# Optimization experiments

Hardware: AMD Instinct MI355X
Metric: run time of the kernel (lower is better)

The kernel has to match this reference:

```python
import jax, jax.numpy as jnp
import numpy as np

B, T, C = 4, 2048, 1024
H, HKV, D = 8, 4, 128          # query heads, kv heads, head dim (C = H*D)
RATIO = 4                       # csa_compress_ratio -> block size
G = T // RATIO                  # number of compressed blocks (T divisible by RATIO)
HI, DI = 8, 64                  # indexer heads / head dim
TOPK = 64                       # index_topk blocks selected per query
ROPE_DIM = 64                   # partial RoPE applied to last ROPE_DIM dims of D
THETA = 160000.0                # compress_rope_theta
RANK = 512                      # grouped output projection rank (o_groups=1)
NEG = -1e30


def rmsnorm(x):
    return x * jax.lax.rsqrt(jnp.mean(jnp.square(x), axis=-1, keepdims=True) + 1e-6)


def rope_tables(pos):
    half = ROPE_DIM // 2
    inv_freq = 1.0 / (THETA ** (jnp.arange(half, dtype=jnp.float32) / half))
    ang = pos.astype(jnp.float32)[:, None] * inv_freq[None, :]   # [P, half]
    return jnp.cos(ang), jnp.sin(ang)


def partial_rope(x, cos, sin):
    # x: [..., P, heads, D]; rotate only the last ROPE_DIM dims
    x_nope, x_rope = x[..., :-ROPE_DIM], x[..., -ROPE_DIM:]
    x1, x2 = jnp.split(x_rope, 2, axis=-1)
    c = cos[:, None, :]  # [P,1,half] broadcast over heads
    s = sin[:, None, :]
    rot = jnp.concatenate([x1 * c - x2 * s, x1 * s + x2 * c], axis=-1)
    return jnp.concatenate([x_nope, rot], axis=-1)


def gated_compress(x, Wk, Wv, Wg, ape, n_head, head_dim):
    # Learned gated softmax pooling over fixed blocks of RATIO tokens.
    k = (x @ Wk).reshape(B, G, RATIO, n_head, head_dim)
    v = (x @ Wv).reshape(B, G, RATIO, n_head, head_dim)
    g = (x @ Wg).reshape(B, G, RATIO, n_head, head_dim) + ape[None, None]
    w = jax.nn.softmax(g, axis=2)
    return (k * w).sum(axis=2), (v * w).sum(axis=2)  # [B,G,h,d]


def setup_inputs() -> dict:
    key = jax.random.key(0)
    ks = jax.random.split(key, 11)
    s = 0.02
    def w(k, shape):
        return jax.random.normal(k, shape, jnp.float32) * s
    return {
        "x": jax.random.normal(ks[0], (B, T, C), jnp.float32),
        "Wq": w(ks[1], (C, H * D)),
        "Wck": w(ks[2], (C, HKV * D)),
        "Wcv": w(ks[3], (C, HKV * D)),
        "Wcg": w(ks[4], (C, HKV * D)),
        "ape_c": jnp.zeros((RATIO, HKV, D), jnp.float32),
        "Wiq": w(ks[5], (C, HI * DI)),
        "Wik": w(ks[6], (C, HI * DI)),
        "Wig": w(ks[7], (C, HI * DI)),
        "ape_i": jnp.zeros((RATIO, HI, DI), jnp.float32),
        "Wa": w(ks[8], (1, RANK, C)),
        "Wb": w(ks[9], (RANK, C)),
    }


def reference(x, Wq, Wck, Wcv, Wcg, ape_c, Wiq, Wik, Wig, ape_i, Wa, Wb):
    group_ends = jnp.arange(RATIO - 1, T, RATIO)                 # [G]
    causal = group_ends[None, :] <= jnp.arange(T)[:, None]       # [T,G]

    # --- LightningIndexer: select TOPK compressed blocks per query token ---
    ki = (x @ Wik).reshape(B, G, RATIO, HI, DI)
    gi = (x @ Wig).reshape(B, G, RATIO, HI, DI) + ape_i[None, None]
    wi = jax.nn.softmax(gi, axis=2)
    ikeys = rmsnorm((ki * wi).sum(axis=2))                       # [B,G,HI,DI]
    iq = rmsnorm((x @ Wiq).reshape(B, T, HI, DI))
    isc = jnp.einsum('bthd,bghd->bhtg', iq, ikeys) * (DI ** -0.5)
    isc = isc.mean(axis=1)                                       # [B,T,G]
    isc = jnp.where(causal[None], isc, NEG)
    sel = jax.lax.top_k(isc, TOPK)[1]                            # [B,T,TOPK]
    mask = jnp.zeros((B, T, G), dtype=bool).at[
        jnp.arange(B)[:, None, None], jnp.arange(T)[None, :, None], sel
    ].set(True)
    mask = mask & causal[None]                                   # [B,T,G]

    # --- Compressed KV + partial RoPE ---
    ck, cv = gated_compress(x, Wck, Wcv, Wcg, ape_c, HKV, D)     # [B,G,HKV,D]
    cos_q, sin_q = rope_tables(jnp.arange(T))
    cos_k, sin_k = rope_tables(group_ends)
    q = partial_rope((x @ Wq).reshape(B, T, H, D), cos_q, sin_q)
    ck = partial_rope(ck, cos_k, sin_k)

    # --- GQA attention over selected compressed blocks ---
    rep = H // HKV
    ck_r = jnp.repeat(ck, rep, axis=2)                           # [B,G,H,D]
    cv_r = jnp.repeat(cv, rep, axis=2)
    scores = jnp.einsum('bthd,bghd->bhtg', q, ck_r) * (D ** -0.5)
    m = mask[:, None]                                            # [B,1,T,G]
    attw = jax.nn.softmax(jnp.where(m, scores, NEG), axis=-1) * m
    attn = jnp.einsum('bhtg,bghd->bthd', attw, cv_r).reshape(B, T, C)

    # --- GroupedOutputProjection (o_groups=1, low-rank) ---
    r = jnp.einsum('btgd,grd->btgr', attn.reshape(B, T, 1, C), Wa).reshape(B, T, RANK)
    return rmsnorm(r) @ Wb
```

## Files before the change

### kernel.cpp

```cpp
#include <hip/hip_runtime.h>
#include <hip/hip_bf16.h>
#include <math.h>

constexpr int kB = 4, kT = 2048, kC = 1024;
constexpr int kH = 8, kHKV = 4, kD = 128;
constexpr int kRATIO = 4, kG = 512;
constexpr int kHI = 8, kDI = 64;
constexpr int kTOPK = 64, kRANK = 512;
constexpr float kTHETA = 160000.0f;
constexpr float kNEG = -1e30f;

constexpr int NTOT = 2560;
constexpr int Q_OFF = 0;
constexpr int CK_OFF = 1024;
constexpr int CV_OFF = 1536;
constexpr int CG_OFF = 2048;

constexpr int PLD = 1536;
constexpr int P_IQ = 0, P_KI = 512, P_GI = 1024;

typedef short short8 __attribute__((ext_vector_type(8)));
typedef float floatx4 __attribute__((ext_vector_type(4)));

__device__ inline float waveReduceSum(float v) {
    #pragma unroll
    for (int m = 32; m > 0; m >>= 1) v += __shfl_xor(v, m, 64);
    return v;
}
__device__ inline double waveReduceSumD(double v) {
    #pragma unroll
    for (int m = 32; m > 0; m >>= 1) v += __shfl_xor(v, m, 64);
    return v;
}
__device__ inline float waveReduceMax(float v) {
    #pragma unroll
    for (int m = 32; m > 0; m >>= 1) v = fmaxf(v, __shfl_xor(v, m, 64));
    return v;
}

__device__ inline unsigned short f2bf(float f) {
    union { float f; unsigned int u; } v; v.f = f;
    unsigned int r = v.u + 0x7FFFu + ((v.u >> 16) & 1u);
    return (unsigned short)(r >> 16);
}
__device__ inline float bf2f(unsigned short h) {
    union { unsigned int u; float f; } v; v.u = ((unsigned int)h) << 16;
    return v.f;
}

__global__ __launch_bounds__(256) void split_rows_kernel(
    const float* __restrict__ in, unsigned short* __restrict__ out,
    int K, int kshift, const float* __restrict__ rowScale)
{
    int idx = blockIdx.x * 256 + threadIdx.x;
    int row = idx >> kshift;
    int kc = (idx & ((1 << kshift) - 1)) << 2;
    float4 v = *(const float4*)(in + (size_t)row * K + kc);
    if (rowScale) {
        float s = rowScale[row];
        v.x *= s; v.y *= s; v.z *= s; v.w *= s;
    }
    unsigned short h[4], l[4];
    float vv[4] = {v.x, v.y, v.z, v.w};
    #pragma unroll
    for (int i = 0; i < 4; ++i) {
        h[i] = f2bf(vv[i]);
        l[i] = f2bf(vv[i] - bf2f(h[i]));
    }
    size_t ob = (size_t)row * (2 * K);
    uint2 hw, lw;
    hw.x = (unsigned)h[0] | ((unsigned)h[1] << 16);
    hw.y = (unsigned)h[2] | ((unsigned)h[3] << 16);
    lw.x = (unsigned)l[0] | ((unsigned)l[1] << 16);
    lw.y = (unsigned)l[2] | ((unsigned)l[3] << 16);
    *(uint2*)(out + ob + kc) = hw;
    *(uint2*)(out + ob + K + kc) = lw;
}

__global__ __launch_bounds__(256) void transpose_split_kernel(
    const float* __restrict__ W, int N, int K, unsigned short* __restrict__ Wt)
{
    __shared__ float Ws[64][68];
    int k0 = blockIdx.x * 64, n0 = blockIdx.y * 64;
    int tid = threadIdx.x;
    #pragma unroll
    for (int it = 0; it < 4; ++it) {
        int krow = (tid >> 4) + it * 16;
        float4 v = *(const float4*)(W + (size_t)(k0 + krow) * N + n0 + (tid & 15) * 4);
        *(float4*)&Ws[krow][(tid & 15) * 4] = v;
    }
    __syncthreads();
    #pragma unroll
    for (int it = 0; it < 2; ++it) {
        int idx = tid + it * 256;
        int nrow = idx >> 3;
        int kc8 = (idx & 7) * 8;
        unsigned short h[8], l[8];
        #pragma unroll
        for (int j = 0; j < 8; ++j) {
            float v = Ws[kc8 + j][nrow];
            h[j] = f2bf(v);
            l[j] = f2bf(v - bf2f(h[j]));
        }
        size_t ob = (size_t)(n0 + nrow) * (2 * K) + k0;
        uint4 hw, lw;
        hw.x = (unsigned)h[0] | ((unsigned)h[1] << 16);
        hw.y = (unsigned)h[2] | ((unsigned)h[3] << 16);
        hw.z = (unsigned)h[4] | ((unsigned)h[5] << 16);
        hw.w = (unsigned)h[6] | ((unsigned)h[7] << 16);
        lw.x = (unsigned)l[0] | ((unsigned)l[1] << 16);
        lw.y = (unsigned)l[2] | ((unsigned)l[3] << 16);
        lw.z = (unsigned)l[4] | ((unsigned)l[5] << 16);
        lw.w = (unsigned)l[6] | ((unsigned)l[7] << 16);
        *(uint4*)(Wt + ob + kc8) = hw;
        *(uint4*)(Wt + ob + K + kc8) = lw;
    }
}

#define TSTRIDE 40

__global__ __launch_bounds__(256) void gemm_mfma_kernel(
    const unsigned short* __restrict__ A,
    const unsigned short* __restrict__ B,
    float* __restrict__ C, int ldc, int Kin)
{
    __shared__ unsigned short As[128 * TSTRIDE];
    __shared__ unsigned short Bs[128 * TSTRIDE];
    const int tid = threadIdx.x;
    const int n0 = blockIdx.x * 128, m0 = blockIdx.y * 128;
    const int w = tid >> 6, lane = tid & 63;
    const int q = lane >> 4, r = lane & 15;
    const int wm = (w & 1) * 64, wn = (w >> 1) * 64;
    const int lda = 2 * Kin, ldb = 2 * Kin;
    const int srow = tid >> 2;
    const int sko = (tid & 3) * 8;

    floatx4 acc[4][4] = {};
    const int KT = 3 * Kin;
    for (int k0 = 0; k0 < KT; k0 += 32) {
        int ka = (k0 < 2 * Kin) ? k0 : k0 - 2 * Kin;
        int kb = (k0 < Kin) ? k0 : k0 - Kin;
        __syncthreads();
        #pragma unroll
        for (int rep = 0; rep < 2; ++rep) {
            int row = srow + rep * 64;
            uint4 av = *(const uint4*)(A + (size_t)(m0 + row) * lda + ka + sko);
            uint4 bv = *(const uint4*)(B + (size_t)(n0 + row) * ldb + kb + sko);
            *(uint4*)&As[row * TSTRIDE + sko] = av;
            *(uint4*)&Bs[row * TSTRIDE + sko] = bv;
        }
        __syncthreads();
        short8 af[4], bf[4];
        #pragma unroll
        for (int i = 0; i < 4; ++i)
            af[i] = *(const short8*)&As[(wm + i * 16 + r) * TSTRIDE + q * 8];
        #pragma unroll
        for (int j = 0; j < 4; ++j)
            bf[j] = *(const short8*)&Bs[(wn + j * 16 + r) * TSTRIDE + q * 8];
        #pragma unroll
        for (int i = 0; i < 4; ++i)
            #pragma unroll
            for (int j = 0; j < 4; ++j)
                acc[i][j] = __builtin_amdgcn_mfma_f32_16x16x32_bf16(
                    af[i], bf[j], acc[i][j], 0, 0, 0);
    }
    #pragma unroll
    for (int i = 0; i < 4; ++i)
        #pragma unroll
        for (int j = 0; j < 4; ++j)
            #pragma unroll
            for (int reg = 0; reg < 4; ++reg)
                C[(size_t)(m0 + wm + i * 16 + q * 4 + reg) * ldc
                  + n0 + wn + j * 16 + r] = acc[i][j][reg];
}

__global__ __launch_bounds__(256) void rope_q_kernel(float* __restrict__ Y)
{
    int idx = blockIdx.x * 256 + threadIdx.x;
    int j = idx & 31;
    int rest = idx >> 5;
    int h = rest & 7;  rest >>= 3;
    int t = rest & (kT - 1);
    int b = rest >> 11;
    size_t base = (size_t)(b * kT + t) * NTOT + Q_OFF + h * kD;
    float inv_freq = powf(kTHETA, -(float)j * (1.0f / 32.0f));
    float ang = (float)t * inv_freq;
    float c = cosf(ang), s = sinf(ang);
    float x1 = Y[base + 64 + j];
    float x2 = Y[base + 96 + j];
    Y[base + 64 + j] = x1 * c - x2 * s;
    Y[base + 96 + j] = x1 * s + x2 * c;
}

__global__ __launch_bounds__(128) void compress_c_kernel(
    const float* __restrict__ Y, const float* __restrict__ ape_c,
    float* __restrict__ ck, float* __restrict__ cv)
{
    int bid = blockIdx.x;
    int h = bid & 3;
    int g = (bid >> 2) & (kG - 1);
    int b = bid >> 11;
    int d = threadIdx.x;
    float kv[kRATIO], vv[kRATIO], gv[kRATIO];
    #pragma unroll
    for (int r = 0; r < kRATIO; ++r) {
        size_t row = (size_t)(b * kT + g * kRATIO + r) * NTOT;
        kv[r] = Y[row + CK_OFF + h * kD + d];
        vv[r] = Y[row + CV_OFF + h * kD + d];
        gv[r] = Y[row + CG_OFF + h * kD + d] + ape_c[(r * kHKV + h) * kD + d];
    }
    float m = fmaxf(fmaxf(gv[0], gv[1]), fmaxf(gv[2], gv[3]));
    float ka = 0.f, va = 0.f, den = 0.f;
    #pragma unroll
    for (int r = 0; r < kRATIO; ++r) {
        float e = expf(gv[r] - m);
        den += e;
        ka += kv[r] * e;
        va += vv[r] * e;
    }
    ka /= den; va /= den;
    size_t obase = ((size_t)(b * kG + g) * kHKV + h) * kD;
    cv[obase + d] = va;
    __shared__ float cks[kD];
    cks[d] = ka;
    __syncthreads();
    int pos = 4 * g + 3;
    float out;
    if (d < 64) {
        out = cks[d];
    } else if (d < 96) {
        int j = d - 64;
        float inv_freq = powf(kTHETA, -(float)j * (1.0f / 32.0f));
        float ang = (float)pos * inv_freq;
        out = cks[d] * cosf(ang) - cks[d + 32] * sinf(ang);
    } else {
        int j = d - 96;
        float inv_freq = powf(kTHETA, -(float)j * (1.0f / 32.0f));
        float ang = (float)pos * inv_freq;
        out = cks[d - 32] * sinf(ang) + cks[d] * cosf(ang);
    }
    ck[obase + d] = out;
}

__global__ __launch_bounds__(256) void concat_w_kernel(
    const float* __restrict__ Wiq, const float* __restrict__ Wik,
    const float* __restrict__ Wig, float* __restrict__ Wcat)
{
    int idx = blockIdx.x * 256 + threadIdx.x;
    int row = idx / 384;
    int col = (idx - row * 384) * 4;
    float4 v;
    if (col < 512)       v = *(const float4*)(Wiq + (size_t)row * 512 + col);
    else if (col < 1024) v = *(const float4*)(Wik + (size_t)row * 512 + col - 512);
    else                 v = *(const float4*)(Wig + (size_t)row * 512 + col - 1024);
    *(float4*)(Wcat + (size_t)row * PLD + col) = v;
}

#define PBM 128
#define PBN 64
#define PBK 16

__global__ __launch_bounds__(256) void proj_f64_kernel(
    const float* __restrict__ x, const float* __restrict__ W,
    double* __restrict__ P)
{
    __shared__ double As[PBK][129];
    __shared__ double Bs[PBK][68];
    const int tid = threadIdx.x;
    const int bx = blockIdx.x, by = blockIdx.y;
    const int tx = tid & 15, ty = tid >> 4;
    const int ar = tid >> 1;
    const int ak = (tid & 1) * 8;
    const int br = tid >> 4;
    const int bc = tid & 15;
    const float* Ap = x + (size_t)(by * PBM + ar) * kC + ak;
    const float* Bp = W + (size_t)br * PLD + bx * PBN + bc;
    double acc[8][4] = {};
    for (int k0 = 0; k0 < kC; k0 += PBK) {
        float4 a0 = *(const float4*)(Ap + k0);
        float4 a1 = *(const float4*)(Ap + k0 + 4);
        const float* bp = Bp + (size_t)k0 * PLD;
        float b0 = bp[0], b1 = bp[16], b2 = bp[32], b3 = bp[48];
        __syncthreads();
        As[ak + 0][ar] = (double)a0.x;
        As[ak + 1][ar] = (double)a0.y;
        As[ak + 2][ar] = (double)a0.z;
        As[ak + 3][ar] = (double)a0.w;
        As[ak + 4][ar] = (double)a1.x;
        As[ak + 5][ar] = (double)a1.y;
        As[ak + 6][ar] = (double)a1.z;
        As[ak + 7][ar] = (double)a1.w;
        Bs[br][bc]      = (double)b0;
        Bs[br][bc + 16] = (double)b1;
        Bs[br][bc + 32] = (double)b2;
        Bs[br][bc + 48] = (double)b3;
        __syncthreads();
        #pragma unroll
        for (int kk = 0; kk < PBK; ++kk) {
            double a[8], b[4];
            #pragma unroll
            for (int i = 0; i < 8; ++i) a[i] = As[kk][ty * 8 + i];
            #pragma unroll
            for (int j = 0; j < 4; ++j) b[j] = Bs[kk][tx + 16 * j];
            #pragma unroll
            for (int i = 0; i < 8; ++i)
                #pragma unroll
                for (int j = 0; j < 4; ++j)
                    acc[i][j] = fma(a[i], b[j], acc[i][j]);
        }
    }
    #pragma unroll
    for (int i = 0; i < 8; ++i)
        #pragma unroll
        for (int j = 0; j < 4; ++j)
            P[(size_t)(by * PBM + ty * 8 + i) * PLD + bx * PBN + tx + 16 * j] = acc[i][j];
}

__global__ __launch_bounds__(64) void gate_i_kernel(
    const double* __restrict__ P, const float* __restrict__ ape_i,
    double* __restrict__ ikeys64)
{
    int bid = blockIdx.x;
    int h = bid & 7;
    int g = (bid >> 3) & (kG - 1);
    int b = bid >> 12;
    int lane = threadIdx.x;
    double kk[kRATIO], gg[kRATIO];
    #pragma unroll
    for (int r = 0; r < kRATIO; ++r) {
        size_t row = (size_t)(b * kT + g * kRATIO + r) * PLD;
        kk[r] = P[row + P_KI + h * kDI + lane];
        gg[r] = P[row + P_GI + h * kDI + lane] + (double)ape_i[(r * kHI + h) * kDI + lane];
    }
    double m = fmax(fmax(gg[0], gg[1]), fmax(gg[2], gg[3]));
    double acc = 0.0, den = 0.0;
    #pragma unroll
    for (int r = 0; r < kRATIO; ++r) {
        double e = exp(gg[r] - m);
        den += e;
        acc += kk[r] * e;
    }
    acc /= den;
    double ss = waveReduceSumD(acc * acc);
    double scale = 1.0 / sqrt(ss * (1.0 / kDI) + 1e-6);
    ikeys64[((size_t)(b * kG + g) * kHI + h) * kDI + lane] = acc * scale;
}

__global__ __launch_bounds__(512) void rmsiq64_kernel(double* __restrict__ P)
{
    int row = blockIdx.x;
    int tid = threadIdx.x;
    double* p = P + (size_t)row * PLD + P_IQ + tid;
    double v = *p;
    double ss = v * v;
    #pragma unroll
    for (int m = 32; m > 0; m >>= 1) ss += __shfl_xor(ss, m, 64);
    double scale = 1.0 / sqrt(ss * (1.0 / kDI) + 1e-6);
    *p = v * scale;
}

#define BM 64
#define BN 64
#define BK 16

__global__ __launch_bounds__(256) void isc_f64_kernel(
    const double* __restrict__ P, const double* __restrict__ ikeys64,
    double* __restrict__ isc64)
{
    __shared__ double As[BK][BM + 1];
    __shared__ double Bs[BK][BN + 4];
    const int tid = threadIdx.x;
    const int bx = blockIdx.x, by = blockIdx.y;
    const int b = by >> 5;
    const int tx = tid & 15, ty = tid >> 4;
    const int arow = tid >> 2;
    const int akq  = (tid & 3) << 2;
    const double* Ap = P + (size_t)(by * BM + arow) * PLD + P_IQ + akq;
    const double* Bp = ikeys64 + (size_t)b * kG * 512 + (size_t)(bx * BN + arow) * 512 + akq;
    double acc[4][4] = {};
    for (int k0 = 0; k0 < 512; k0 += BK) {
        double a0 = Ap[k0], a1 = Ap[k0 + 1], a2 = Ap[k0 + 2], a3 = Ap[k0 + 3];
        double b0 = Bp[k0], b1 = Bp[k0 + 1], b2 = Bp[k0 + 2], b3 = Bp[k0 + 3];
        __syncthreads();
        As[akq + 0][arow] = a0; As[akq + 1][arow] = a1;
        As[akq + 2][arow] = a2; As[akq + 3][arow] = a3;
        Bs[akq + 0][arow] = b0; Bs[akq + 1][arow] = b1;
        Bs[akq + 2][arow] = b2; Bs[akq + 3][arow] = b3;
        __syncthreads();
        #pragma unroll
        for (int kk = 0; kk < BK; ++kk) {
            double a[4];
            #pragma unroll
            for (int i = 0; i < 4; ++i) a[i] = As[kk][ty * 4 + i];
            #pragma unroll
            for (int j = 0; j < 4; ++j) {
                double bv = Bs[kk][tx * 4 + j];
                #pragma unroll
                for (int i = 0; i < 4; ++i)
                    acc[i][j] = fma(a[i], bv, acc[i][j]);
            }
        }
    }
    #pragma unroll
    for (int i = 0; i < 4; ++i)
        #pragma unroll
        for (int j = 0; j < 4; ++j)
            isc64[(size_t)(by * BM + ty * 4 + i) * kG + bx * BN + tx * 4 + j] =
                acc[i][j] * (1.0 / 64.0);
}

__global__ __launch_bounds__(256) void topk_kernel(
    const double* __restrict__ isc, int* __restrict__ sel, int* __restrict__ cnt)
{
    int bt = blockIdx.x;
    int t = bt & (kT - 1);
    int tid = threadIdx.x;
    __shared__ unsigned long long sk[kG];
    const double* row = isc + (size_t)bt * kG;
    for (int g = tid; g < kG; g += 256) {
        bool causal = (4 * g + 3) <= t;
        unsigned long long key;
        if (causal) {
            union { double d; unsigned long long u; } v; v.d = row[g];
            unsigned long long b = v.u;
            key = (b >> 63) ? ~b : (b | 0x8000000000000000ULL);
            key = (key & ~511ULL) | (unsigned long long)(511 - g);
        } else {
            key = (unsigned long long)(511 - g);
        }
        sk[g] = key;
    }
    __syncthreads();
    for (int k = 2; k <= kG; k <<= 1) {
        for (int j = k >> 1; j > 0; j >>= 1) {
            #pragma unroll 2
            for (int i = tid; i < kG; i += 256) {
                int l = i ^ j;
                if (l > i) {
                    unsigned long long ki = sk[i], kl = sk[l];
                    bool l_first = kl > ki;
                    bool desc = ((i & k) == 0);
                    if (desc ? l_first : !l_first) {
                        sk[i] = kl; sk[l] = ki;
                    }
                }
            }
            __syncthreads();
        }
    }
    int count = (t >= 3) ? (((t - 3) >> 2) + 1) : 0;
    int n = count < kTOPK ? count : kTOPK;
    if (tid < kTOPK)
        sel[(size_t)bt * kTOPK + tid] =
            (tid < n) ? (511 - (int)(sk[tid] & 511ULL)) : 0;
    if (tid == 0) cnt[bt] = n;
}

__global__ __launch_bounds__(64) void attn_kernel(
    const float* __restrict__ Y, const float* __restrict__ ck,
    const float* __restrict__ cv, const int* __restrict__ sel,
    const int* __restrict__ cnt, unsigned short* __restrict__ acat)
{
    int bid = blockIdx.x;
    int h = bid & 7;
    int row = bid >> 3;
    int b = row >> 11;
    int lane = threadIdx.x;
    __shared__ float qs[kD];
    __shared__ float ws[kTOPK];
    __shared__ int gs[kTOPK];
    const float* qp = Y + (size_t)row * NTOT + Q_OFF + h * kD;
    qs[lane] = qp[lane];
    qs[lane + 64] = qp[lane + 64];
    __syncthreads();
    int n = cnt[row];
    unsigned short* outp = acat + (size_t)row * 2048 + h * kD;
    float acc0 = 0.f, acc1 = 0.f;
    if (n > 0) {
        int kvh = h >> 1;
        float score = kNEG;
        int g = 0;
        if (lane < n) {
            g = sel[(size_t)row * kTOPK + lane];
            const float* ckp = ck + ((size_t)(b * kG + g) * kHKV + kvh) * kD;
            float s = 0.f;
            #pragma unroll
            for (int d = 0; d < kD; d += 4) {
                float4 c4 = *(const float4*)(ckp + d);
                s += qs[d] * c4.x + qs[d + 1] * c4.y + qs[d + 2] * c4.z + qs[d + 3] * c4.w;
            }
            score = s * 0.08838834764831845f;
        }
        float m = waveReduceMax(score);
        float p = (lane < n) ? expf(score - m) : 0.f;
        float sum = waveReduceSum(p);
        float w = p / sum;
        ws[lane] = w;
        gs[lane] = g;
        __syncthreads();
        for (int j = 0; j < n; ++j) {
            float wj = ws[j];
            const float* cvp = cv + ((size_t)(b * kG + gs[j]) * kHKV + kvh) * kD;
            acc0 = fmaf(wj, cvp[lane], acc0);
            acc1 = fmaf(wj, cvp[lane + 64], acc1);
        }
    }
    unsigned short h0 = f2bf(acc0), h1 = f2bf(acc1);
    outp[lane] = h0;
    outp[lane + 64] = h1;
    outp[1024 + lane] = f2bf(acc0 - bf2f(h0));
    outp[1024 + lane + 64] = f2bf(acc1 - bf2f(h1));
}

__global__ __launch_bounds__(64) void rms_rows_kernel(
    const float* __restrict__ R, float* __restrict__ scale)
{
    int row = blockIdx.x;
    int lane = threadIdx.x;
    const float* p = R + (size_t)row * kRANK;
    float s = 0.f;
    #pragma unroll
    for (int i = 0; i < kRANK / 64; ++i) {
        float v = p[lane + i * 64];
        s = fmaf(v, v, s);
    }
    s = waveReduceSum(s);
    if (lane == 0) scale[row] = 1.0f / sqrtf(s * (1.0f / kRANK) + 1e-6f);
}

extern "C" void kernel_launch(void* const* d_in, const int* in_sizes, int n_in,
                              void* d_out, int out_size, void* d_ws, size_t ws_size,
                              hipStream_t stream)
{
    const float* x    = (const float*)d_in[0];
    const float* Wq   = (const float*)d_in[1];
    const float* Wck  = (const float*)d_in[2];
    const float* Wcv  = (const float*)d_in[3];
    const float* Wcg  = (const float*)d_in[4];
    const float* ape_c= (const float*)d_in[5];
    const float* Wiq  = (const float*)d_in[6];
    const float* Wik  = (const float*)d_in[7];
    const float* Wig  = (const float*)d_in[8];
    const float* ape_i= (const float*)d_in[9];
    const float* Wa   = (const float*)d_in[10];
    const float* Wb   = (const float*)d_in[11];
    float* out = (float*)d_out;

    const int M = kB * kT;

    char* p = (char*)d_ws;
    double* P       = (double*)p;              p += (size_t)M * PLD * 8;
    double* ikeys64 = (double*)p;              p += (size_t)kB * kG * 512 * 8;
    double* isc64   = (double*)p;              p += (size_t)M * kG * 8;
    float* ck       = (float*)p;               p += (size_t)kB * kG * kHKV * kD * 4;
    float* cv       = (float*)p;               p += (size_t)kB * kG * kHKV * kD * 4;
    float* rbuf     = (float*)p;               p += (size_t)M * kRANK * 4;
    float* rscale   = (float*)p;               p += (size_t)M * 4;
    int* sel        = (int*)p;                 p += (size_t)M * kTOPK * 4;
    int* cnt        = (int*)p;                 p += (size_t)M * 4;
    unsigned short* xcat  = (unsigned short*)p; p += (size_t)M * 2048 * 2;
    unsigned short* Wtall = (unsigned short*)p; p += (size_t)NTOT * 2048 * 2;
    unsigned short* Wat   = (unsigned short*)p; p += (size_t)kRANK * 2048 * 2;
    unsigned short* Wbt   = (unsigned short*)p; p += (size_t)kC * 1024 * 2;
    float* Wcat     = (float*)p;               p += (size_t)kC * PLD * 4;
    float* Y = (float*)P;
    unsigned short* acat  = xcat;
    unsigned short* rncat = (unsigned short*)isc64;

    concat_w_kernel<<<(kC * PLD / 4) / 256, 256, 0, stream>>>(Wiq, Wik, Wig, Wcat);
    proj_f64_kernel<<<dim3(PLD / PBN, M / PBM), 256, 0, stream>>>(x, Wcat, P);
    gate_i_kernel<<<kB * kG * kHI, 64, 0, stream>>>(P, ape_i, ikeys64);
    rmsiq64_kernel<<<M, 512, 0, stream>>>(P);
    isc_f64_kernel<<<dim3(kG / BN, M / BM), 256, 0, stream>>>(P, ikeys64, isc64);
    topk_kernel<<<kB * kT, 256, 0, stream>>>(isc64, sel, cnt);

    split_rows_kernel<<<(size_t)M * kC / 4 / 256, 256, 0, stream>>>(
        x, xcat, kC, 8, nullptr);
    transpose_split_kernel<<<dim3(kC / 64, 1024 / 64), 256, 0, stream>>>(
        Wq, 1024, kC, Wtall + (size_t)Q_OFF * 2048);
    transpose_split_kernel<<<dim3(kC / 64, 512 / 64), 256, 0, stream>>>(
        Wck, 512, kC, Wtall + (size_t)CK_OFF * 2048);
    transpose_split_kernel<<<dim3(kC / 64, 512 / 64), 256, 0, stream>>>(
        Wcv, 512, kC, Wtall + (size_t)CV_OFF * 2048);
    transpose_split_kernel<<<dim3(kC / 64, 512 / 64), 256, 0, stream>>>(
        Wcg, 512, kC, Wtall + (size_t)CG_OFF * 2048);

    gemm_mfma_kernel<<<dim3(NTOT / 128, M / 128), 256, 0, stream>>>(
        xcat, Wtall, Y, NTOT, kC);

    rope_q_kernel<<<(kB * kT * kH * 32) / 256, 256, 0, stream>>>(Y);
    compress_c_kernel<<<kB * kG * kHKV, 128, 0, stream>>>(Y, ape_c, ck, cv);

    attn_kernel<<<kB * kT * kH, 64, 0, stream>>>(Y, ck, cv, sel, cnt, acat);

    split_rows_kernel<<<(size_t)kRANK * kC / 4 / 256, 256, 0, stream>>>(
        Wa, Wat, kC, 8, nullptr);
    gemm_mfma_kernel<<<dim3(kRANK / 128, M / 128), 256, 0, stream>>>(
        acat, Wat, rbuf, kRANK, kC);

    rms_rows_kernel<<<M, 64, 0, stream>>>(rbuf, rscale);
    split_rows_kernel<<<(size_t)M * kRANK / 4 / 256, 256, 0, stream>>>(
        rbuf, rncat, kRANK, 7, rscale);
    transpose_split_kernel<<<dim3(kRANK / 64, kC / 64), 256, 0, stream>>>(
        Wb, kC, kRANK, Wbt);
    gemm_mfma_kernel<<<dim3(kC / 128, M / 128), 256, 0, stream>>>(
        rncat, Wbt, out, kC, kRANK);

    (void)in_sizes; (void)n_in; (void)out_size; (void)ws_size;
}
```

Before: 1.567 ms.

## Enlarge f64 GEMM tiles and share KV loads across GQA head pairs in attention

The fp64 projection GEMM tile grows from 128x64 to 128x128 with an 8x8 register accumulator per thread. The fp64 indexer-score GEMM tile grows from 64x64 to 64x128 with a 4x8 accumulator, and both get occupancy hints in their launch bounds. Attention now runs one 256-thread block per token, with each wave covering both query heads of a KV head, so each ck/cv load serves two heads and softmax weights pass through shuffles instead of shared memory. The larger tiles raise register pressure and cut the block count, which may lower occupancy.

```diff
diff --git a/kernel.cpp b/kernel.cpp
--- a/kernel.cpp
+++ b/kernel.cpp
@@ -257,15 +257,15 @@
 }
 
 #define PBM 128
-#define PBN 64
+#define PBN 128
 #define PBK 16
 
-__global__ __launch_bounds__(256) void proj_f64_kernel(
+__global__ __launch_bounds__(256, 2) void proj_f64_kernel(
     const float* __restrict__ x, const float* __restrict__ W,
     double* __restrict__ P)
 {
-    __shared__ double As[PBK][129];
-    __shared__ double Bs[PBK][68];
+    __shared__ double As[PBK][PBM + 1];
+    __shared__ double Bs[PBK][PBN + 8];
     const int tid = threadIdx.x;
     const int bx = blockIdx.x, by = blockIdx.y;
     const int tx = tid & 15, ty = tid >> 4;
@@ -275,12 +275,14 @@
     const int bc = tid & 15;
     const float* Ap = x + (size_t)(by * PBM + ar) * kC + ak;
     const float* Bp = W + (size_t)br * PLD + bx * PBN + bc;
-    double acc[8][4] = {};
+    double acc[8][8] = {};
     for (int k0 = 0; k0 < kC; k0 += PBK) {
         float4 a0 = *(const float4*)(Ap + k0);
         float4 a1 = *(const float4*)(Ap + k0 + 4);
         const float* bp = Bp + (size_t)k0 * PLD;
-        float b0 = bp[0], b1 = bp[16], b2 = bp[32], b3 = bp[48];
+        float bv[8];
+        #pragma unroll
+        for (int i = 0; i < 8; ++i) bv[i] = bp[16 * i];
         __syncthreads();
         As[ak + 0][ar] = (double)a0.x;
         As[ak + 1][ar] = (double)a0.y;
@@ -290,29 +292,27 @@
         As[ak + 5][ar] = (double)a1.y;
         As[ak + 6][ar] = (double)a1.z;
         As[ak + 7][ar] = (double)a1.w;
-        Bs[br][bc]      = (double)b0;
-        Bs[br][bc + 16] = (double)b1;
-        Bs[br][bc + 32] = (double)b2;
-        Bs[br][bc + 48] = (double)b3;
+        #pragma unroll
+        for (int i = 0; i < 8; ++i) Bs[br][bc + 16 * i] = (double)bv[i];
         __syncthreads();
         #pragma unroll
         for (int kk = 0; kk < PBK; ++kk) {
-            double a[8], b[4];
+            double a[8], b[8];
             #pragma unroll
             for (int i = 0; i < 8; ++i) a[i] = As[kk][ty * 8 + i];
             #pragma unroll
-            for (int j = 0; j < 4; ++j) b[j] = Bs[kk][tx + 16 * j];
+            for (int j = 0; j < 8; ++j) b[j] = Bs[kk][tx + 16 * j];
             #pragma unroll
             for (int i = 0; i < 8; ++i)
                 #pragma unroll
-                for (int j = 0; j < 4; ++j)
+                for (int j = 0; j < 8; ++j)
                     acc[i][j] = fma(a[i], b[j], acc[i][j]);
         }
     }
     #pragma unroll
     for (int i = 0; i < 8; ++i)
         #pragma unroll
-        for (int j = 0; j < 4; ++j)
+        for (int j = 0; j < 8; ++j)
             P[(size_t)(by * PBM + ty * 8 + i) * PLD + bx * PBN + tx + 16 * j] = acc[i][j];
 }
 
@@ -359,53 +359,55 @@
     *p = v * scale;
 }
 
-#define BM 64
-#define BN 64
-#define BK 16
-
-__global__ __launch_bounds__(256) void isc_f64_kernel(
+__global__ __launch_bounds__(256, 2) void isc_f64_kernel(
     const double* __restrict__ P, const double* __restrict__ ikeys64,
     double* __restrict__ isc64)
 {
-    __shared__ double As[BK][BM + 1];
-    __shared__ double Bs[BK][BN + 4];
+    __shared__ double As[16][65];
+    __shared__ double Bs[16][136];
     const int tid = threadIdx.x;
     const int bx = blockIdx.x, by = blockIdx.y;
     const int b = by >> 5;
     const int tx = tid & 15, ty = tid >> 4;
-    const int arow = tid >> 2;
-    const int akq  = (tid & 3) << 2;
-    const double* Ap = P + (size_t)(by * BM + arow) * PLD + P_IQ + akq;
-    const double* Bp = ikeys64 + (size_t)b * kG * 512 + (size_t)(bx * BN + arow) * 512 + akq;
-    double acc[4][4] = {};
-    for (int k0 = 0; k0 < 512; k0 += BK) {
-        double a0 = Ap[k0], a1 = Ap[k0 + 1], a2 = Ap[k0 + 2], a3 = Ap[k0 + 3];
-        double b0 = Bp[k0], b1 = Bp[k0 + 1], b2 = Bp[k0 + 2], b3 = Bp[k0 + 3];
+    const int ar = tid >> 2;
+    const int ak = (tid & 3) * 4;
+    const int bn = tid >> 1;
+    const int bk = (tid & 1) * 8;
+    const double* Ap = P + (size_t)(by * 64 + ar) * PLD + P_IQ + ak;
+    const double* Bp = ikeys64 + (size_t)b * kG * 512
+                     + (size_t)(bx * 128 + bn) * 512 + bk;
+    double acc[4][8] = {};
+    for (int k0 = 0; k0 < 512; k0 += 16) {
+        double av[4], bv[8];
+        #pragma unroll
+        for (int i = 0; i < 4; ++i) av[i] = Ap[k0 + i];
+        #pragma unroll
+        for (int i = 0; i < 8; ++i) bv[i] = Bp[k0 + i];
         __syncthreads();
-        As[akq + 0][arow] = a0; As[akq + 1][arow] = a1;
-        As[akq + 2][arow] = a2; As[akq + 3][arow] = a3;
-        Bs[akq + 0][arow] = b0; Bs[akq + 1][arow] = b1;
-        Bs[akq + 2][arow] = b2; Bs[akq + 3][arow] = b3;
+        #pragma unroll
+        for (int i = 0; i < 4; ++i) As[ak + i][ar] = av[i];
+        #pragma unroll
+        for (int i = 0; i < 8; ++i) Bs[bk + i][bn] = bv[i];
         __syncthreads();
         #pragma unroll
-        for (int kk = 0; kk < BK; ++kk) {
-            double a[4];
+        for (int kk = 0; kk < 16; ++kk) {
+            double a[4], b2[8];
             #pragma unroll
             for (int i = 0; i < 4; ++i) a[i] = As[kk][ty * 4 + i];
             #pragma unroll
-            for (int j = 0; j < 4; ++j) {
-                double bv = Bs[kk][tx * 4 + j];
+            for (int j = 0; j < 8; ++j) b2[j] = Bs[kk][tx + 16 * j];
+            #pragma unroll
+            for (int i = 0; i < 4; ++i)
                 #pragma unroll
-                for (int i = 0; i < 4; ++i)
-                    acc[i][j] = fma(a[i], bv, acc[i][j]);
-            }
+                for (int j = 0; j < 8; ++j)
+                    acc[i][j] = fma(a[i], b2[j], acc[i][j]);
         }
     }
     #pragma unroll
     for (int i = 0; i < 4; ++i)
         #pragma unroll
-        for (int j = 0; j < 4; ++j)
-            isc64[(size_t)(by * BM + ty * 4 + i) * kG + bx * BN + tx * 4 + j] =
+        for (int j = 0; j < 8; ++j)
+            isc64[(size_t)(by * 64 + ty * 4 + i) * kG + bx * 128 + tx + 16 * j] =
                 acc[i][j] * (1.0 / 64.0);
 }
 
@@ -456,60 +458,65 @@
     if (tid == 0) cnt[bt] = n;
 }
 
-__global__ __launch_bounds__(64) void attn_kernel(
+__global__ __launch_bounds__(256) void attn_kernel(
     const float* __restrict__ Y, const float* __restrict__ ck,
     const float* __restrict__ cv, const int* __restrict__ sel,
     const int* __restrict__ cnt, unsigned short* __restrict__ acat)
 {
-    int bid = blockIdx.x;
-    int h = bid & 7;
-    int row = bid >> 3;
+    int row = blockIdx.x;
     int b = row >> 11;
-    int lane = threadIdx.x;
-    __shared__ float qs[kD];
-    __shared__ float ws[kTOPK];
-    __shared__ int gs[kTOPK];
-    const float* qp = Y + (size_t)row * NTOT + Q_OFF + h * kD;
-    qs[lane] = qp[lane];
-    qs[lane + 64] = qp[lane + 64];
+    int tid = threadIdx.x;
+    int w = tid >> 6, lane = tid & 63;
+    __shared__ float qs[kC];
+    const float* qp = Y + (size_t)row * NTOT + Q_OFF;
+    *(float4*)&qs[tid * 4] = *(const float4*)&qp[tid * 4];
     __syncthreads();
     int n = cnt[row];
-    unsigned short* outp = acat + (size_t)row * 2048 + h * kD;
-    float acc0 = 0.f, acc1 = 0.f;
-    if (n > 0) {
-        int kvh = h >> 1;
-        float score = kNEG;
-        int g = 0;
-        if (lane < n) {
-            g = sel[(size_t)row * kTOPK + lane];
-            const float* ckp = ck + ((size_t)(b * kG + g) * kHKV + kvh) * kD;
-            float s = 0.f;
-            #pragma unroll
-            for (int d = 0; d < kD; d += 4) {
-                float4 c4 = *(const float4*)(ckp + d);
-                s += qs[d] * c4.x + qs[d + 1] * c4.y + qs[d + 2] * c4.z + qs[d + 3] * c4.w;
-            }
-            score = s * 0.08838834764831845f;
+    int h0 = 2 * w, h1 = 2 * w + 1, kvh = w;
+    float sc0 = kNEG, sc1 = kNEG;
+    int g = 0;
+    if (lane < n) {
+        g = sel[(size_t)row * kTOPK + lane];
+        const float* ckp = ck + ((size_t)(b * kG + g) * kHKV + kvh) * kD;
+        float s0 = 0.f, s1 = 0.f;
+        #pragma unroll
+        for (int d = 0; d < kD; d += 4) {
+            float4 c4 = *(const float4*)(ckp + d);
+            float4 q0 = *(const float4*)&qs[h0 * kD + d];
+            float4 q1 = *(const float4*)&qs[h1 * kD + d];
+            s0 += q0.x * c4.x + q0.y * c4.y + q0.z * c4.z + q0.w * c4.w;
+            s1 += q1.x * c4.x + q1.y * c4.y + q1.z * c4.z + q1.w * c4.w;
         }
-        float m = waveReduceMax(score);
-        float p = (lane < n) ? expf(score - m) : 0.f;
-        float sum = waveReduceSum(p);
-        float w = p / sum;
-        ws[lane] = w;
-        gs[lane] = g;
-        __syncthreads();
-        for (int j = 0; j < n; ++j) {
-            float wj = ws[j];
-            const float* cvp = cv + ((size_t)(b * kG + gs[j]) * kHKV + kvh) * kD;
-            acc0 = fmaf(wj, cvp[lane], acc0);
-            acc1 = fmaf(wj, cvp[lane + 64], acc1);
-        }
-    }
-    unsigned short h0 = f2bf(acc0), h1 = f2bf(acc1);
-    outp[lane] = h0;
-    outp[lane + 64] = h1;
-    outp[1024 + lane] = f2bf(acc0 - bf2f(h0));
-    outp[1024 + lane + 64] = f2bf(acc1 - bf2f(h1));
+        sc0 = s0 * 0.08838834764831845f;
+        sc1 = s1 * 0.08838834764831845f;
+    }
+    float m0 = waveReduceMax(sc0), m1 = waveReduceMax(sc1);
+    float p0 = (lane < n) ? expf(sc0 - m0) : 0.f;
+    float p1 = (lane < n) ? expf(sc1 - m1) : 0.f;
+    float sum0 = waveReduceSum(p0), sum1 = waveReduceSum(p1);
+    float w0 = p0 / sum0, w1 = p1 / sum1;
+    float acc00 = 0.f, acc01 = 0.f, acc10 = 0.f, acc11 = 0.f;
+    for (int j = 0; j < n; ++j) {
+        float wj0 = __shfl(w0, j, 64);
+        float wj1 = __shfl(w1, j, 64);
+        int gj = __shfl(g, j, 64);
+        const float* cvp = cv + ((size_t)(b * kG + gj) * kHKV + kvh) * kD;
+        float v0 = cvp[lane], v1 = cvp[lane + 64];
+        acc00 = fmaf(wj0, v0, acc00);
+        acc01 = fmaf(wj0, v1, acc01);
+        acc10 = fmaf(wj1, v0, acc10);
+        acc11 = fmaf(wj1, v1, acc11);
+    }
+    unsigned short* outp0 = acat + (size_t)row * 2048 + h0 * kD;
+    unsigned short* outp1 = acat + (size_t)row * 2048 + h1 * kD;
+    unsigned short a0 = f2bf(acc00), a1 = f2bf(acc01);
+    unsigned short b0 = f2bf(acc10), b1 = f2bf(acc11);
+    outp0[lane] = a0;           outp0[lane + 64] = a1;
+    outp0[1024 + lane] = f2bf(acc00 - bf2f(a0));
+    outp0[1024 + lane + 64] = f2bf(acc01 - bf2f(a1));
+    outp1[lane] = b0;           outp1[lane + 64] = b1;
+    outp1[1024 + lane] = f2bf(acc10 - bf2f(b0));
+    outp1[1024 + lane + 64] = f2bf(acc11 - bf2f(b1));
 }
 
 __global__ __launch_bounds__(64) void rms_rows_kernel(
@@ -571,7 +578,7 @@
     proj_f64_kernel<<<dim3(PLD / PBN, M / PBM), 256, 0, stream>>>(x, Wcat, P);
     gate_i_kernel<<<kB * kG * kHI, 64, 0, stream>>>(P, ape_i, ikeys64);
     rmsiq64_kernel<<<M, 512, 0, stream>>>(P);
-    isc_f64_kernel<<<dim3(kG / BN, M / BM), 256, 0, stream>>>(P, ikeys64, isc64);
+    isc_f64_kernel<<<dim3(kG / 128, M / 64), 256, 0, stream>>>(P, ikeys64, isc64);
     topk_kernel<<<kB * kT, 256, 0, stream>>>(isc64, sel, cnt);
 
     split_rows_kernel<<<(size_t)M * kC / 4 / 256, 256, 0, stream>>>(
@@ -591,7 +598,7 @@
     rope_q_kernel<<<(kB * kT * kH * 32) / 256, 256, 0, stream>>>(Y);
     compress_c_kernel<<<kB * kG * kHKV, 128, 0, stream>>>(Y, ape_c, ck, cv);
 
-    attn_kernel<<<kB * kT * kH, 64, 0, stream>>>(Y, ck, cv, sel, cnt, acat);
+    attn_kernel<<<kB * kT, 256, 0, stream>>>(Y, ck, cv, sel, cnt, acat);
 
     split_rows_kernel<<<(size_t)kRANK * kC / 4 / 256, 256, 0, stream>>>(
         Wa, Wat, kC, 8, nullptr);
```

Measured after the change: 1.459 ms. -6.9%, faster.
